# Optimization experiments

Measured on AMD Instinct MI355X. Metric: run time of the kernel, lower is better.

The kernel has to match this reference:

```python
import jax, jax.numpy as jnp
import numpy as np

LEAKY_SLOPE = 0.01

def bilinear_interpolate(grid, coords):
    # grid: [H, W, C]; coords: [N, 2] in [0,1] (x, y order as in torch code)
    H = grid.shape[0] - 1
    W = grid.shape[1] - 1
    fx = coords[:, 0] * W
    fy = coords[:, 1] * H
    x0 = fx.astype(jnp.int32)
    y0 = fy.astype(jnp.int32)
    xf = jnp.mod(fx, 1.0)
    yf = jnp.mod(fy, 1.0)
    x1 = jnp.minimum(x0 + 1, W)
    y1 = jnp.minimum(y0 + 1, H)
    tl = grid[y0, x0]  # [N, C]
    tr = grid[y0, x1]
    bl = grid[y1, x0]
    br = grid[y1, x1]
    xf = xf[:, None]
    yf = yf[:, None]
    top = (1.0 - xf) * tl + xf * tr
    bot = (1.0 - xf) * bl + xf * br
    return (1.0 - yf) * top + yf * bot


def setup_inputs() -> dict:
    key = jax.random.key(0)
    ks = jax.random.split(key, 10)
    N = 2097152
    pos = jax.random.uniform(ks[0], (N, 2), dtype=jnp.float32)
    dir = jax.random.uniform(ks[1], (N, 2), dtype=jnp.float32)
    pos_grid = jax.random.normal(ks[2], (256, 256, 3), dtype=jnp.float32) * 10.0
    dir_grid = jax.random.normal(ks[3], (256, 256, 3), dtype=jnp.float32) * 10.0
    # Linear layers: PyTorch default init U(-1/sqrt(fan_in), 1/sqrt(fan_in))
    def linear(kw, kb, fan_in, fan_out):
        bound = 1.0 / np.sqrt(fan_in)
        W = jax.random.uniform(kw, (fan_out, fan_in), minval=-bound, maxval=bound, dtype=jnp.float32)
        b = jax.random.uniform(kb, (fan_out,), minval=-bound, maxval=bound, dtype=jnp.float32)
        return W, b
    W1, b1 = linear(ks[4], ks[5], 6, 64)
    W2, b2 = linear(ks[6], ks[7], 64, 64)
    W3, b3 = linear(ks[8], ks[9], 64, 1)
    return {"pos": pos, "dir": dir, "pos_grid": pos_grid, "dir_grid": dir_grid,
            "W1": W1, "b1": b1, "W2": W2, "b2": b2, "W3": W3, "b3": b3}


def reference(pos, dir, pos_grid, dir_grid, W1, b1, W2, b2, W3, b3):
    pos_feat = jax.lax.stop_gradient(bilinear_interpolate(pos_grid, pos))  # .detach() in torch
    dir_feat = jax.lax.stop_gradient(bilinear_interpolate(dir_grid, dir))
    x = jnp.concatenate([pos_feat, dir_feat], axis=1)  # [N, 6]
    x = jax.nn.leaky_relu(x @ W1.T + b1, LEAKY_SLOPE)
    x = jax.nn.leaky_relu(x @ W2.T + b2, LEAKY_SLOPE)
    return jax.nn.sigmoid(x @ W3.T + b3)  # [N, 1]
```

## Files before the change

kernel.cpp:

```cpp
#include <hip/hip_runtime.h>
#include <hip/hip_bf16.h>
#include <math.h>


#define NTHREADS 256
#define NB 4
#define LSTRIDE 72
#define WAVE_L (64 * LSTRIDE)

typedef __attribute__((ext_vector_type(8))) short bf16x8;
typedef __attribute__((ext_vector_type(4))) float f32x4;
typedef __attribute__((ext_vector_type(4))) int i32x4;
typedef __attribute__((ext_vector_type(2))) int i32x2;

static __device__ __forceinline__ short f2bf(float f) {
    return __builtin_bit_cast(short, __float2bfloat16(f));
}
static __device__ __forceinline__ int pk2(float lo, float hi) {
    unsigned short l = (unsigned short)f2bf(lo);
    unsigned short h = (unsigned short)f2bf(hi);
    return (int)(((unsigned int)h << 16) | (unsigned int)l);
}

static __device__ __forceinline__ void bilerp3(const float* __restrict__ g,
                                               float px, float py, float* f) {
    float fx = px * 255.0f;
    float fy = py * 255.0f;
    int x0 = (int)fx;
    int y0 = (int)fy;
    float xf = fx - floorf(fx);
    float yf = fy - floorf(fy);
    int x1 = min(x0 + 1, 255);
    int y1 = min(y0 + 1, 255);
    const float* r00 = g + (y0 * 256 + x0) * 3;
    const float* r01 = g + (y0 * 256 + x1) * 3;
    const float* r10 = g + (y1 * 256 + x0) * 3;
    const float* r11 = g + (y1 * 256 + x1) * 3;
#pragma unroll
    for (int ch = 0; ch < 3; ++ch) {
        float tl = r00[ch], tr = r01[ch], bl = r10[ch], br = r11[ch];
        float top = fmaf(xf, tr - tl, tl);
        float bot = fmaf(xf, br - bl, bl);
        f[ch] = fmaf(yf, bot - top, top);
    }
}

__global__ __launch_bounds__(NTHREADS, 3) void mlp_mfma_kernel(
    const float* __restrict__ pos, const float* __restrict__ dir,
    const float* __restrict__ pos_grid, const float* __restrict__ dir_grid,
    const float* __restrict__ W1, const float* __restrict__ b1,
    const float* __restrict__ W2, const float* __restrict__ b2,
    const float* __restrict__ W3, const float* __restrict__ b3,
    float* __restrict__ out) {
    __shared__ short lds_L[4 * WAVE_L];
    __shared__ int lds_F[4 * 2 * 64 * 4];

    const int w = threadIdx.x >> 6;
    const int lane = threadIdx.x & 63;
    const int c = lane & 15;
    const int q = lane >> 4;

    short* L = lds_L + w * WAVE_L;
    int* FB = lds_F + w * (2 * 64 * 4);

    bf16x8 A1f[4];
#pragma unroll
    for (int mt = 0; mt < 4; ++mt) {
        int f = mt * 16 + c;
        bf16x8 t;
#pragma unroll
        for (int j = 0; j < 8; ++j) {
            float v = 0.0f;
            if (q == 0) {
                if (j < 6) v = W1[f * 6 + j];
                else if (j == 6) v = b1[f];
            }
            t[j] = f2bf(v);
        }
        A1f[mt] = t;
    }
    bf16x8 A2f[2][4];
#pragma unroll
    for (int kt = 0; kt < 2; ++kt)
#pragma unroll
        for (int mt = 0; mt < 4; ++mt) {
            int n2 = mt * 16 + c;
            int k0 = kt * 32 + q * 8;
            bf16x8 t;
#pragma unroll
            for (int j = 0; j < 8; ++j) t[j] = f2bf(W2[n2 * 64 + k0 + j]);
            A2f[kt][mt] = t;
        }
    f32x4 ci[4], w3q[4];
#pragma unroll
    for (int ft = 0; ft < 4; ++ft)
#pragma unroll
        for (int r = 0; r < 4; ++r) {
            ci[ft][r] = b2[ft * 16 + q * 4 + r];
            w3q[ft][r] = W3[ft * 16 + q * 4 + r];
        }
    const float b3s = b3[0];
    const int dbias = pk2(1.0f, 0.0f);

    const long wave_global = (long)blockIdx.x * 4 + w;
    const long base0 = wave_global * (64L * NB);
    const f32x4 zacc = {0.f, 0.f, 0.f, 0.f};

    {
        float2 pp = ((const float2*)pos)[base0 + lane];
        float2 dd = ((const float2*)dir)[base0 + lane];
        float feat[6];
        bilerp3(pos_grid, pp.x, pp.y, feat);
        bilerp3(dir_grid, dd.x, dd.y, feat + 3);
        i32x4 dv;
        dv[0] = pk2(feat[0], feat[1]);
        dv[1] = pk2(feat[2], feat[3]);
        dv[2] = pk2(feat[4], feat[5]);
        dv[3] = dbias;
        *(i32x4*)(FB + lane * 4) = dv;
    }

#pragma unroll 1
    for (int ib = 0; ib < NB; ++ib) {
        const long base = base0 + ib * 64;
        const int cur = ib & 1;

#pragma unroll
        for (int pt = 0; pt < 4; ++pt) {
            const int row = pt * 16 + c;
            i32x4 bi = *(const i32x4*)(FB + cur * 256 + row * 4);
            bf16x8 bfrag = __builtin_bit_cast(bf16x8, bi);
            f32x4 a1[4];
#pragma unroll
            for (int mt = 0; mt < 4; ++mt)
                a1[mt] = __builtin_amdgcn_mfma_f32_16x16x32_bf16(
                    A1f[mt], bfrag, zacc, 0, 0, 0);
#pragma unroll
            for (int mt = 0; mt < 4; ++mt) {
                float l0 = a1[mt][0], l1 = a1[mt][1];
                float l2 = a1[mt][2], l3 = a1[mt][3];
                l0 = fmaxf(l0, 0.01f * l0);
                l1 = fmaxf(l1, 0.01f * l1);
                l2 = fmaxf(l2, 0.01f * l2);
                l3 = fmaxf(l3, 0.01f * l3);
                i32x2 wv;
                wv[0] = pk2(l0, l1);
                wv[1] = pk2(l2, l3);
                *(i32x2*)(L + row * LSTRIDE + mt * 16 + q * 4) = wv;
            }
        }

        {
            const long nbase = (ib + 1 < NB) ? (base + 64) : base;
            float2 pp = ((const float2*)pos)[nbase + lane];
            float2 dd = ((const float2*)dir)[nbase + lane];
            float feat[6];
            bilerp3(pos_grid, pp.x, pp.y, feat);
            bilerp3(dir_grid, dd.x, dd.y, feat + 3);
            i32x4 dv;
            dv[0] = pk2(feat[0], feat[1]);
            dv[1] = pk2(feat[2], feat[3]);
            dv[2] = pk2(feat[4], feat[5]);
            dv[3] = dbias;
            *(i32x4*)(FB + (cur ^ 1) * 256 + lane * 4) = dv;
        }

        float s[4];
#pragma unroll
        for (int pt = 0; pt < 4; ++pt) {
            const int row = pt * 16 + c;
            bf16x8 h0 = *(const bf16x8*)(L + row * LSTRIDE + q * 8);
            bf16x8 h1 = *(const bf16x8*)(L + row * LSTRIDE + 32 + q * 8);
            float t = 0.0f;
#pragma unroll
            for (int ft = 0; ft < 4; ++ft) {
                f32x4 t0 = __builtin_amdgcn_mfma_f32_16x16x32_bf16(
                    A2f[0][ft], h0, ci[ft], 0, 0, 0);
                f32x4 a2 = __builtin_amdgcn_mfma_f32_16x16x32_bf16(
                    A2f[1][ft], h1, t0, 0, 0, 0);
#pragma unroll
                for (int r = 0; r < 4; ++r) {
                    float x = a2[r];
                    x = fmaxf(x, 0.01f * x);
                    t = fmaf(x, w3q[ft][r], t);
                }
            }
            t += __shfl_xor(t, 16, 64);
            t += __shfl_xor(t, 32, 64);
            s[pt] = t;
        }

        float sa = (q & 1) ? s[1] : s[0];
        float sb = (q & 1) ? s[3] : s[2];
        float v = (q & 2) ? sb : sa;
        v += b3s;
        v = 1.0f / (1.0f + __expf(-v));
        out[base + q * 16 + c] = v;
    }
}

extern "C" void kernel_launch(void* const* d_in, const int* in_sizes, int n_in,
                              void* d_out, int out_size, void* d_ws,
                              size_t ws_size, hipStream_t stream) {
    const float* pos = (const float*)d_in[0];
    const float* dir = (const float*)d_in[1];
    const float* pos_grid = (const float*)d_in[2];
    const float* dir_grid = (const float*)d_in[3];
    const float* W1 = (const float*)d_in[4];
    const float* b1 = (const float*)d_in[5];
    const float* W2 = (const float*)d_in[6];
    const float* b2 = (const float*)d_in[7];
    const float* W3 = (const float*)d_in[8];
    const float* b3 = (const float*)d_in[9];
    float* out = (float*)d_out;

    const int n = in_sizes[0] / 2;
    const int batches = n / 64;
    const int waves = batches / NB;
    const int blocks = waves / 4;

    mlp_mfma_kernel<<<blocks, NTHREADS, 0, stream>>>(
        pos, dir, pos_grid, dir_grid, W1, b1, W2, b2, W3, b3, out);
}
```

Baseline: 168.8 us.

## Pre-pack grids into bf16 corner patches and software-pipeline gathers two batches ahead

Adds a pre-pass kernel that packs each grid cell's four bilinear corners into a contiguous 32-byte bf16 patch. The main kernel then fetches a whole patch with one 16B and one 8B load instead of twelve scattered fp32 loads. Patch loads are issued two batches ahead and coordinate loads further ahead, to hide gather latency behind the MFMA work. The cost is two extra small launches, rounding the grid corners to bf16 before interpolation (a precision loss), and higher register pressure from the pipelined patch buffers.

```diff
diff --git a/kernel.cpp b/kernel.cpp
--- a/kernel.cpp
+++ b/kernel.cpp
@@ -21,24 +21,56 @@
     unsigned short h = (unsigned short)f2bf(hi);
     return (int)(((unsigned int)h << 16) | (unsigned int)l);
 }
-
-static __device__ __forceinline__ void bilerp3(const float* __restrict__ g,
-                                               float px, float py, float* f) {
+static __device__ __forceinline__ float bflo(int u) {
+    return __builtin_bit_cast(float, u << 16);
+}
+static __device__ __forceinline__ float bfhi(int u) {
+    return __builtin_bit_cast(float, (int)(u & 0xffff0000));
+}
+
+__global__ __launch_bounds__(256) void make_patches(
+    const float* __restrict__ g, int* __restrict__ pout) {
+    int id = blockIdx.x * 256 + threadIdx.x;
+    int y0 = id >> 8, x0 = id & 255;
+    int x1 = min(x0 + 1, 255), y1 = min(y0 + 1, 255);
+    const float* tl = g + (y0 * 256 + x0) * 3;
+    const float* tr = g + (y0 * 256 + x1) * 3;
+    const float* bl = g + (y1 * 256 + x0) * 3;
+    const float* br = g + (y1 * 256 + x1) * 3;
+    i32x4 u0;
+    i32x2 u1;
+    u0[0] = pk2(tl[0], bl[0]);
+    u0[1] = pk2(tl[1], bl[1]);
+    u0[2] = pk2(tl[2], bl[2]);
+    u0[3] = pk2(tr[0], br[0]);
+    u1[0] = pk2(tr[1], br[1]);
+    u1[1] = pk2(tr[2], br[2]);
+    *(i32x4*)(pout + id * 8) = u0;
+    *(i32x2*)(pout + id * 8 + 4) = u1;
+}
+
+static __device__ __forceinline__ void patch_issue(
+    const int* __restrict__ tab, float px, float py, int* P, float& xf,
+    float& yf) {
     float fx = px * 255.0f;
     float fy = py * 255.0f;
     int x0 = (int)fx;
     int y0 = (int)fy;
-    float xf = fx - floorf(fx);
-    float yf = fy - floorf(fy);
-    int x1 = min(x0 + 1, 255);
-    int y1 = min(y0 + 1, 255);
-    const float* r00 = g + (y0 * 256 + x0) * 3;
-    const float* r01 = g + (y0 * 256 + x1) * 3;
-    const float* r10 = g + (y1 * 256 + x0) * 3;
-    const float* r11 = g + (y1 * 256 + x1) * 3;
+    xf = fx - floorf(fx);
+    yf = fy - floorf(fy);
+    int idx = (y0 << 8) | x0;
+    i32x4 a = *(const i32x4*)(tab + idx * 8);
+    i32x2 b = *(const i32x2*)(tab + idx * 8 + 4);
+    P[0] = a[0]; P[1] = a[1]; P[2] = a[2];
+    P[3] = a[3]; P[4] = b[0]; P[5] = b[1];
+}
+
+static __device__ __forceinline__ void patch_lerp(const int* P, float xf,
+                                                  float yf, float* f) {
 #pragma unroll
     for (int ch = 0; ch < 3; ++ch) {
-        float tl = r00[ch], tr = r01[ch], bl = r10[ch], br = r11[ch];
+        float tl = bflo(P[ch]), bl = bfhi(P[ch]);
+        float tr = bflo(P[ch + 3]), br = bfhi(P[ch + 3]);
         float top = fmaf(xf, tr - tl, tl);
         float bot = fmaf(xf, br - bl, bl);
         f[ch] = fmaf(yf, bot - top, top);
@@ -47,7 +79,7 @@
 
 __global__ __launch_bounds__(NTHREADS, 3) void mlp_mfma_kernel(
     const float* __restrict__ pos, const float* __restrict__ dir,
-    const float* __restrict__ pos_grid, const float* __restrict__ dir_grid,
+    const int* __restrict__ patP, const int* __restrict__ patD,
     const float* __restrict__ W1, const float* __restrict__ b1,
     const float* __restrict__ W2, const float* __restrict__ b2,
     const float* __restrict__ W3, const float* __restrict__ b3,
@@ -105,25 +137,56 @@
     const long wave_global = (long)blockIdx.x * 4 + w;
     const long base0 = wave_global * (64L * NB);
     const f32x4 zacc = {0.f, 0.f, 0.f, 0.f};
+    const float2* pos2 = (const float2*)pos;
+    const float2* dir2 = (const float2*)dir;
+
+    int PA[12], PB[12];
+    float frA[4], frB[4];
+    float2 cp2, cd2, cp3, cd3;
 
     {
-        float2 pp = ((const float2*)pos)[base0 + lane];
-        float2 dd = ((const float2*)dir)[base0 + lane];
+        float2 c0p = pos2[base0 + lane], c0d = dir2[base0 + lane];
+        float2 c1p = pos2[base0 + 64 + lane], c1d = dir2[base0 + 64 + lane];
+        cp2 = pos2[base0 + 128 + lane];
+        cd2 = dir2[base0 + 128 + lane];
+        cp3 = pos2[base0 + 192 + lane];
+        cd3 = dir2[base0 + 192 + lane];
+        int P0_[12];
+        float fr0[4];
+        patch_issue(patP, c0p.x, c0p.y, P0_, fr0[0], fr0[1]);
+        patch_issue(patD, c0d.x, c0d.y, P0_ + 6, fr0[2], fr0[3]);
         float feat[6];
-        bilerp3(pos_grid, pp.x, pp.y, feat);
-        bilerp3(dir_grid, dd.x, dd.y, feat + 3);
+        patch_lerp(P0_, fr0[0], fr0[1], feat);
+        patch_lerp(P0_ + 6, fr0[2], fr0[3], feat + 3);
         i32x4 dv;
         dv[0] = pk2(feat[0], feat[1]);
         dv[1] = pk2(feat[2], feat[3]);
         dv[2] = pk2(feat[4], feat[5]);
         dv[3] = dbias;
         *(i32x4*)(FB + lane * 4) = dv;
+        patch_issue(patP, c1p.x, c1p.y, PA, frA[0], frA[1]);
+        patch_issue(patD, c1d.x, c1d.y, PA + 6, frA[2], frA[3]);
     }
 
 #pragma unroll 1
     for (int ib = 0; ib < NB; ++ib) {
         const long base = base0 + ib * 64;
         const int cur = ib & 1;
+
+        patch_issue(patP, cp2.x, cp2.y, PB, frB[0], frB[1]);
+        patch_issue(patD, cd2.x, cd2.y, PB + 6, frB[2], frB[3]);
+
+        {
+            float feat[6];
+            patch_lerp(PA, frA[0], frA[1], feat);
+            patch_lerp(PA + 6, frA[2], frA[3], feat + 3);
+            i32x4 dv;
+            dv[0] = pk2(feat[0], feat[1]);
+            dv[1] = pk2(feat[2], feat[3]);
+            dv[2] = pk2(feat[4], feat[5]);
+            dv[3] = dbias;
+            *(i32x4*)(FB + (cur ^ 1) * 256 + lane * 4) = dv;
+        }
 
 #pragma unroll
         for (int pt = 0; pt < 4; ++pt) {
@@ -150,21 +213,6 @@
             }
         }
 
-        {
-            const long nbase = (ib + 1 < NB) ? (base + 64) : base;
-            float2 pp = ((const float2*)pos)[nbase + lane];
-            float2 dd = ((const float2*)dir)[nbase + lane];
-            float feat[6];
-            bilerp3(pos_grid, pp.x, pp.y, feat);
-            bilerp3(dir_grid, dd.x, dd.y, feat + 3);
-            i32x4 dv;
-            dv[0] = pk2(feat[0], feat[1]);
-            dv[1] = pk2(feat[2], feat[3]);
-            dv[2] = pk2(feat[4], feat[5]);
-            dv[3] = dbias;
-            *(i32x4*)(FB + (cur ^ 1) * 256 + lane * 4) = dv;
-        }
-
         float s[4];
 #pragma unroll
         for (int pt = 0; pt < 4; ++pt) {
@@ -196,6 +244,15 @@
         v += b3s;
         v = 1.0f / (1.0f + __expf(-v));
         out[base + q * 16 + c] = v;
+
+#pragma unroll
+        for (int i2 = 0; i2 < 12; ++i2) PA[i2] = PB[i2];
+        frA[0] = frB[0]; frA[1] = frB[1]; frA[2] = frB[2]; frA[3] = frB[3];
+        cp2 = cp3;
+        cd2 = cd3;
+        int mb = min(ib + 4, NB - 1);
+        cp3 = pos2[base0 + mb * 64 + lane];
+        cd3 = dir2[base0 + mb * 64 + lane];
     }
 }
 
@@ -214,11 +271,17 @@
     const float* b3 = (const float*)d_in[9];
     float* out = (float*)d_out;
 
+    int* patP = (int*)d_ws;
+    int* patD = patP + 65536 * 8;
+
+    make_patches<<<256, 256, 0, stream>>>(pos_grid, patP);
+    make_patches<<<256, 256, 0, stream>>>(dir_grid, patD);
+
     const int n = in_sizes[0] / 2;
     const int batches = n / 64;
     const int waves = batches / NB;
     const int blocks = waves / 4;
 
     mlp_mfma_kernel<<<blocks, NTHREADS, 0, stream>>>(
-        pos, dir, pos_grid, dir_grid, W1, b1, W2, b2, W3, b3, out);
-}
+        pos, dir, patP, patD, W1, b1, W2, b2, W3, b3, out);
+}
```

New measurement: 160.7 us. 4.8% less time.
